# Kernel optimization log

Measured on AMD Instinct MI355X. Metric: run time of the kernel, lower is better.

Reference implementation:

```python
import jax, jax.numpy as jnp
import numpy as np
import math

H = 16
D_MODEL = 1024
D_K = D_MODEL // H
B, S = 2, 2048


def setup_inputs() -> dict:
    key = jax.random.key(0)
    ks = jax.random.split(key, 12)
    s = 1.0 / math.sqrt(D_MODEL)
    inp = {
        "Q": jax.random.normal(ks[0], (B, S, D_MODEL), jnp.float32),
        "K": jax.random.normal(ks[1], (B, S, D_MODEL), jnp.float32),
        "V": jax.random.normal(ks[2], (B, S, D_MODEL), jnp.float32),
        # causal mask: True = masked (future positions)
        "mask": jnp.triu(jnp.ones((S, S), bool), k=1)[None, None, :, :],
        "Wq": jax.random.normal(ks[3], (D_MODEL, D_MODEL), jnp.float32) * s,
        "bq": jax.random.normal(ks[4], (D_MODEL,), jnp.float32) * s,
        "Wk": jax.random.normal(ks[5], (D_MODEL, D_MODEL), jnp.float32) * s,
        "bk": jax.random.normal(ks[6], (D_MODEL,), jnp.float32) * s,
        "Wv": jax.random.normal(ks[7], (D_MODEL, D_MODEL), jnp.float32) * s,
        "bv": jax.random.normal(ks[8], (D_MODEL,), jnp.float32) * s,
        "Wo": jax.random.normal(ks[9], (D_MODEL, D_MODEL), jnp.float32) * s,
        "bo": jax.random.normal(ks[10], (D_MODEL,), jnp.float32) * s,
    }
    return inp


def reference(Q, K, V, mask, Wq, bq, Wk, bk, Wv, bv, Wo, bo):
    b, s, _ = Q.shape
    # torch Linear: y = x @ W^T + b
    q = (Q @ Wq.T + bq).reshape(b, s, H, D_K).transpose(0, 2, 1, 3)  # [b,h,s,dk]
    k = (K @ Wk.T + bk).reshape(b, s, H, D_K).transpose(0, 2, 1, 3)
    v = (V @ Wv.T + bv).reshape(b, s, H, D_K).transpose(0, 2, 1, 3)
    scores = jnp.einsum("bhqd,bhkd->bhqk", q, k) / jnp.sqrt(jnp.float32(D_K))
    scores = jnp.where(mask, jnp.float32(-1e9), scores)
    weights = jax.nn.softmax(scores, axis=-1)
    sdpa = jnp.einsum("bhqk,bhkd->bhqd", weights, v)
    sdpa = sdpa.transpose(0, 2, 1, 3).reshape(b, s, D_MODEL)
    return sdpa @ Wo.T + bo
```

## Files before the change

kernel.cpp:

```cpp
#include <hip/hip_runtime.h>
#include <hip/hip_bf16.h>
#include <stdint.h>

#define NH     16
#define DMODEL 1024
#define DKH    64
#define BATCH  2
#define SEQ    2048
#define MROWS  (BATCH * SEQ)

typedef __hip_bfloat16 bf16;
typedef __attribute__((ext_vector_type(8))) short bf16x8;
typedef __attribute__((ext_vector_type(4))) float f32x4;

#define AS3(p) ((__attribute__((address_space(3))) void*)(p))
#define AS1(p) ((const __attribute__((address_space(1))) void*)(p))

__device__ __forceinline__ f32x4 mfma16(bf16x8 a, bf16x8 b, f32x4 c) {
    return __builtin_amdgcn_mfma_f32_16x16x32_bf16(a, b, c, 0, 0, 0);
}

struct CvtArgs {
    const float* src[7];
    bf16* dst[7];
    int n[7];
};

__global__ __launch_bounds__(256) void cvt_kernel(CvtArgs a) {
    const int r = blockIdx.y;
    const int i = ((int)blockIdx.x * 256 + (int)threadIdx.x) * 4;
    if (i >= a.n[r]) return;
    const float4 v = *reinterpret_cast<const float4*>(a.src[r] + i);
    union { bf16 t[4]; uint2 u; } tu;
    tu.t[0] = __float2bfloat16(v.x);
    tu.t[1] = __float2bfloat16(v.y);
    tu.t[2] = __float2bfloat16(v.z);
    tu.t[3] = __float2bfloat16(v.w);
    *reinterpret_cast<uint2*>(reinterpret_cast<char*>(a.dst[r]) + (size_t)i * 2) = tu.u;
}

struct GemmArgs {
    const bf16* A[3];
    const bf16* W[3];
    const float* bias[3];
    void* out[3];
    int mode0;
};

__global__ __launch_bounds__(256) void gemm_bt(GemmArgs ga) {
    const int z = blockIdx.z;
    const int mode = ga.mode0 + z;
    const bf16* __restrict__ A = ga.A[z];
    const bf16* __restrict__ W = ga.W[z];
    const float* __restrict__ bias = ga.bias[z];

    __shared__ bf16 lA[128 * 64];
    __shared__ bf16 lB[128 * 64];

    const int tid = (int)threadIdx.x;
    const int w = tid >> 6;
    const int l = tid & 63;
    const int quad = l >> 4;
    const int sl = l & 15;
    const int wr = w >> 1;
    const int wc = w & 1;
    const int m0 = (int)blockIdx.x * 128;
    const int n0 = (int)blockIdx.y * 128;

    f32x4 acc[4][4];
#pragma unroll
    for (int i = 0; i < 4; ++i)
#pragma unroll
        for (int j = 0; j < 4; ++j)
            acc[i][j] = (f32x4){0.f, 0.f, 0.f, 0.f};

    for (int kt = 0; kt < 16; ++kt) {
        const int k0 = kt * 64;
        __syncthreads();
#pragma unroll
        for (int j = 0; j < 4; ++j) {
            const int row = w * 32 + j * 8 + (l >> 3);
            const int col = ((l & 7) ^ (row & 7)) * 8;
            __builtin_amdgcn_global_load_lds(AS1(A + (size_t)(m0 + row) * DMODEL + k0 + col),
                                             AS3((char*)lA + (w * 4 + j) * 1024), 16, 0, 0);
            __builtin_amdgcn_global_load_lds(AS1(W + (size_t)(n0 + row) * DMODEL + k0 + col),
                                             AS3((char*)lB + (w * 4 + j) * 1024), 16, 0, 0);
        }
        asm volatile("s_waitcnt vmcnt(0)" ::: "memory");
        __syncthreads();

        bf16x8 af[4][2], bfr[4][2];
#pragma unroll
        for (int i = 0; i < 4; ++i) {
            const int row = wr * 64 + i * 16 + sl;
#pragma unroll
            for (int ks = 0; ks < 2; ++ks) {
                const int cb = (ks * 64 + quad * 16) ^ ((row & 7) << 4);
                af[i][ks] = *reinterpret_cast<const bf16x8*>((const char*)lA + row * 128 + cb);
            }
        }
#pragma unroll
        for (int j = 0; j < 4; ++j) {
            const int row = wc * 64 + j * 16 + sl;
#pragma unroll
            for (int ks = 0; ks < 2; ++ks) {
                const int cb = (ks * 64 + quad * 16) ^ ((row & 7) << 4);
                bfr[j][ks] = *reinterpret_cast<const bf16x8*>((const char*)lB + row * 128 + cb);
            }
        }
#pragma unroll
        for (int ks = 0; ks < 2; ++ks)
#pragma unroll
            for (int i = 0; i < 4; ++i)
#pragma unroll
                for (int j = 0; j < 4; ++j)
                    acc[i][j] = mfma16(af[i][ks], bfr[j][ks], acc[i][j]);
    }

#pragma unroll
    for (int j = 0; j < 4; ++j) {
        const int n = n0 + wc * 64 + j * 16 + sl;
        const float bj = bias[n];
        const int h = n >> 6;
        const int dk = n & 63;
#pragma unroll
        for (int i = 0; i < 4; ++i) {
#pragma unroll
            for (int r = 0; r < 4; ++r) {
                const int m = m0 + wr * 64 + i * 16 + quad * 4 + r;
                const int b = m >> 11;
                const int s = m & (SEQ - 1);
                const float v = acc[i][j][r] + bj;
                if (mode == 0) {
                    ((bf16*)ga.out[z])[((size_t)(b * NH + h) * SEQ + s) * DKH + dk] =
                        __float2bfloat16(v * 0.125f);
                } else if (mode == 1) {
                    ((bf16*)ga.out[z])[((size_t)(b * NH + h) * SEQ + s) * DKH + dk] =
                        __float2bfloat16(v);
                } else if (mode == 2) {
                    ((bf16*)ga.out[z])[((size_t)(b * NH + h) * DKH + dk) * SEQ + s] =
                        __float2bfloat16(v);
                } else {
                    ((float*)ga.out[z])[(size_t)m * DMODEL + n] = v;
                }
            }
        }
    }
}

__global__ __launch_bounds__(256, 2) void attn_kernel(const bf16* __restrict__ q,
                                                      const bf16* __restrict__ k,
                                                      const bf16* __restrict__ vT,
                                                      bf16* __restrict__ o) {
    __shared__ bf16 kbuf[2][64 * 64];
    __shared__ bf16 vbuf[2][64 * 64];
    __shared__ bf16 pl[4][16][72];

    const int tid = (int)threadIdx.x;
    const int w = tid >> 6;
    const int l = tid & 63;
    const int quad = l >> 4;
    const int sl = l & 15;

    const int L = (int)blockIdx.x;
    const int j0 = L >> 3;
    const int bh = (L & 7) * 4 + (j0 >> 4);
    const int x = j0 & 15;
    const int b = bh >> 4;
    const int h = bh & 15;

    const bf16* qb = q + (size_t)bh * SEQ * DKH;
    const bf16* kb = k + (size_t)bh * SEQ * DKH;
    const bf16* vb = vT + (size_t)bh * DKH * SEQ;

    const int sq = w * 2;
    int cur = 0;

    auto stage = [&](int kv0, int buf) {
#pragma unroll
        for (int jj = 0; jj < 2; ++jj) {
            const int qq = sq + jj;
            const int row = qq * 8 + (l >> 3);
            const int col = ((l & 7) ^ (row & 7)) * 8;
            __builtin_amdgcn_global_load_lds(AS1(kb + (size_t)(kv0 + row) * DKH + col),
                                             AS3((char*)kbuf[buf] + qq * 1024), 16, 0, 0);
            __builtin_amdgcn_global_load_lds(AS1(vb + (size_t)row * SEQ + kv0 + col),
                                             AS3((char*)vbuf[buf] + qq * 1024), 16, 0, 0);
        }
    };

    for (int t = 0; t < 2; ++t) {
        const int qt = t ? (31 - x) : x;
        const int q0 = qt * 64 + w * 16;

        bf16x8 aq[2];
#pragma unroll
        for (int ks = 0; ks < 2; ++ks)
            aq[ks] = *reinterpret_cast<const bf16x8*>(
                qb + (size_t)(q0 + sl) * DKH + ks * 32 + quad * 8);

        float m_[4], ls[4];
        f32x4 o_[4];
#pragma unroll
        for (int r = 0; r < 4; ++r) { m_[r] = -3.0e38f; ls[r] = 0.f; }
#pragma unroll
        for (int dc = 0; dc < 4; ++dc) o_[dc] = (f32x4){0.f, 0.f, 0.f, 0.f};

        const int nt = qt + 1;
        stage(0, cur);

        for (int tile = 0; tile < nt; ++tile) {
            const int kv0 = tile * 64;
            asm volatile("s_waitcnt vmcnt(0)" ::: "memory");
            __syncthreads();
            if (tile + 1 < nt) stage((tile + 1) * 64, cur ^ 1);

            bf16x8 kf[4][2];
#pragma unroll
            for (int kc = 0; kc < 4; ++kc) {
                const int row = kc * 16 + sl;
#pragma unroll
                for (int ds = 0; ds < 2; ++ds) {
                    const int cb = (ds * 64 + quad * 16) ^ ((row & 7) << 4);
                    kf[kc][ds] = *reinterpret_cast<const bf16x8*>(
                        (const char*)kbuf[cur] + row * 128 + cb);
                }
            }

            f32x4 sc[4];
#pragma unroll
            for (int kc = 0; kc < 4; ++kc) sc[kc] = (f32x4){0.f, 0.f, 0.f, 0.f};
#pragma unroll
            for (int ds = 0; ds < 2; ++ds)
#pragma unroll
                for (int kc = 0; kc < 4; ++kc)
                    sc[kc] = mfma16(aq[ds], kf[kc][ds], sc[kc]);

            if (kv0 + 63 > q0) {
#pragma unroll
                for (int kc = 0; kc < 4; ++kc) {
                    const int key = kv0 + kc * 16 + sl;
#pragma unroll
                    for (int r = 0; r < 4; ++r) {
                        const int qr = q0 + quad * 4 + r;
                        if (key > qr) sc[kc][r] = -1.0e30f;
                    }
                }
            }

            float tm[4];
#pragma unroll
            for (int r = 0; r < 4; ++r)
                tm[r] = fmaxf(fmaxf(sc[0][r], sc[1][r]), fmaxf(sc[2][r], sc[3][r]));
#pragma unroll
            for (int off = 1; off < 16; off <<= 1)
#pragma unroll
                for (int r = 0; r < 4; ++r)
                    tm[r] = fmaxf(tm[r], __shfl_xor(tm[r], off, 64));

            float resc[4];
#pragma unroll
            for (int r = 0; r < 4; ++r) {
                const float mn = fmaxf(m_[r], tm[r]);
                resc[r] = __expf(m_[r] - mn);
                m_[r] = mn;
            }
            float tsum[4] = {0.f, 0.f, 0.f, 0.f};
#pragma unroll
            for (int kc = 0; kc < 4; ++kc)
#pragma unroll
                for (int r = 0; r < 4; ++r) {
                    const float p = __expf(sc[kc][r] - m_[r]);
                    sc[kc][r] = p;
                    tsum[r] += p;
                }
#pragma unroll
            for (int off = 1; off < 16; off <<= 1)
#pragma unroll
                for (int r = 0; r < 4; ++r)
                    tsum[r] += __shfl_xor(tsum[r], off, 64);
#pragma unroll
            for (int r = 0; r < 4; ++r) ls[r] = ls[r] * resc[r] + tsum[r];
#pragma unroll
            for (int dc = 0; dc < 4; ++dc)
#pragma unroll
                for (int r = 0; r < 4; ++r)
                    o_[dc][r] *= resc[r];

#pragma unroll
            for (int kc = 0; kc < 4; ++kc)
#pragma unroll
                for (int r = 0; r < 4; ++r)
                    pl[w][quad * 4 + r][kc * 16 + sl] = __float2bfloat16(sc[kc][r]);
            asm volatile("s_waitcnt lgkmcnt(0)" ::: "memory");

            bf16x8 pa[2];
#pragma unroll
            for (int ks = 0; ks < 2; ++ks)
                pa[ks] = *reinterpret_cast<const bf16x8*>(
                    reinterpret_cast<const char*>(&pl[w][0][0]) + sl * 144 + (ks * 32 + quad * 8) * 2);

            bf16x8 bv[4][2];
#pragma unroll
            for (int dc = 0; dc < 4; ++dc) {
                const int row = dc * 16 + sl;
#pragma unroll
                for (int ks = 0; ks < 2; ++ks) {
                    const int cb = (ks * 64 + quad * 16) ^ ((row & 7) << 4);
                    bv[dc][ks] = *reinterpret_cast<const bf16x8*>(
                        (const char*)vbuf[cur] + row * 128 + cb);
                }
            }
#pragma unroll
            for (int ks = 0; ks < 2; ++ks)
#pragma unroll
                for (int dc = 0; dc < 4; ++dc)
                    o_[dc] = mfma16(pa[ks], bv[dc][ks], o_[dc]);

            cur ^= 1;
        }

#pragma unroll
        for (int r = 0; r < 4; ++r) {
            const float inv = 1.f / ls[r];
            const int row = q0 + quad * 4 + r;
#pragma unroll
            for (int dc = 0; dc < 4; ++dc)
                o[((size_t)(b * SEQ + row)) * DMODEL + h * DKH + dc * 16 + sl] =
                    __float2bfloat16(o_[dc][r] * inv);
        }
    }
}

extern "C" void kernel_launch(void* const* d_in, const int* in_sizes, int n_in,
                              void* d_out, int out_size, void* d_ws, size_t ws_size,
                              hipStream_t stream) {
    const float* Q  = (const float*)d_in[0];
    const float* K  = (const float*)d_in[1];
    const float* V  = (const float*)d_in[2];
    const float* Wq = (const float*)d_in[4];
    const float* bq = (const float*)d_in[5];
    const float* Wk = (const float*)d_in[6];
    const float* bk = (const float*)d_in[7];
    const float* Wv = (const float*)d_in[8];
    const float* bv = (const float*)d_in[9];
    const float* Wo = (const float*)d_in[10];
    const float* bo = (const float*)d_in[11];

    char* ws = (char*)d_ws;
    const size_t MB = 1024 * 1024;
    bf16* Qb   = (bf16*)(ws + 0 * MB);
    bf16* Kb   = (bf16*)(ws + 8 * MB);
    bf16* Vb   = (bf16*)(ws + 16 * MB);
    bf16* Wqb  = (bf16*)(ws + 24 * MB);
    bf16* Wkb  = (bf16*)(ws + 26 * MB);
    bf16* Wvb  = (bf16*)(ws + 28 * MB);
    bf16* Wob  = (bf16*)(ws + 30 * MB);
    bf16* qh   = (bf16*)(ws + 32 * MB);
    bf16* kh   = (bf16*)(ws + 40 * MB);
    bf16* vTh  = (bf16*)(ws + 48 * MB);
    bf16* sdpa = (bf16*)(ws + 0 * MB);

    CvtArgs ca;
    ca.src[0] = Q;  ca.dst[0] = Qb;  ca.n[0] = MROWS * DMODEL;
    ca.src[1] = K;  ca.dst[1] = Kb;  ca.n[1] = MROWS * DMODEL;
    ca.src[2] = V;  ca.dst[2] = Vb;  ca.n[2] = MROWS * DMODEL;
    ca.src[3] = Wq; ca.dst[3] = Wqb; ca.n[3] = DMODEL * DMODEL;
    ca.src[4] = Wk; ca.dst[4] = Wkb; ca.n[4] = DMODEL * DMODEL;
    ca.src[5] = Wv; ca.dst[5] = Wvb; ca.n[5] = DMODEL * DMODEL;
    ca.src[6] = Wo; ca.dst[6] = Wob; ca.n[6] = DMODEL * DMODEL;
    cvt_kernel<<<dim3(4096, 7, 1), 256, 0, stream>>>(ca);

    GemmArgs g1;
    g1.A[0] = Qb; g1.W[0] = Wqb; g1.bias[0] = bq; g1.out[0] = qh;
    g1.A[1] = Kb; g1.W[1] = Wkb; g1.bias[1] = bk; g1.out[1] = kh;
    g1.A[2] = Vb; g1.W[2] = Wvb; g1.bias[2] = bv; g1.out[2] = vTh;
    g1.mode0 = 0;
    gemm_bt<<<dim3(MROWS / 128, DMODEL / 128, 3), 256, 0, stream>>>(g1);

    attn_kernel<<<dim3(512, 1, 1), 256, 0, stream>>>(qh, kh, vTh, sdpa);

    GemmArgs g2;
    g2.A[0] = sdpa; g2.W[0] = Wob; g2.bias[0] = bo; g2.out[0] = d_out;
    g2.A[1] = sdpa; g2.W[1] = Wob; g2.bias[1] = bo; g2.out[1] = d_out;
    g2.A[2] = sdpa; g2.W[2] = Wob; g2.bias[2] = bo; g2.out[2] = d_out;
    g2.mode0 = 3;
    gemm_bt<<<dim3(MROWS / 128, DMODEL / 128, 1), 256, 0, stream>>>(g2);
}
```

Baseline: 273.8 us.

## Stage 128-key KV tiles in attention and coalesce transposed V projection stores

After: 266.4 us. -2.7%, faster.

```diff
diff --git a/kernel.cpp b/kernel.cpp
--- a/kernel.cpp
+++ b/kernel.cpp
@@ -54,8 +54,9 @@
     const bf16* __restrict__ W = ga.W[z];
     const float* __restrict__ bias = ga.bias[z];
 
-    __shared__ bf16 lA[128 * 64];
-    __shared__ bf16 lB[128 * 64];
+    __shared__ __align__(16) char smem[32768];
+    bf16* lA = (bf16*)smem;
+    bf16* lB = (bf16*)(smem + 16384);
 
     const int tid = (int)threadIdx.x;
     const int w = tid >> 6;
@@ -117,6 +118,41 @@
                     acc[i][j] = mfma16(af[i][ks], bfr[j][ks], acc[i][j]);
     }
 
+    if (mode == 2) {
+        bf16* tr = (bf16*)smem;
+        const int b = m0 >> 11;
+        const int s0 = m0 & (SEQ - 1);
+        bf16* outp = (bf16*)ga.out[z];
+#pragma unroll
+        for (int jh = 0; jh < 2; ++jh) {
+            __syncthreads();
+#pragma unroll
+            for (int j2 = 0; j2 < 2; ++j2) {
+                const int j = jh * 2 + j2;
+                const int n = n0 + wc * 64 + j * 16 + sl;
+                const float bj = bias[n];
+                const int row_l = wc * 32 + j2 * 16 + sl;
+#pragma unroll
+                for (int i = 0; i < 4; ++i)
+#pragma unroll
+                    for (int r = 0; r < 4; ++r) {
+                        const int s_l = wr * 64 + i * 16 + quad * 4 + r;
+                        tr[row_l * 130 + s_l] = __float2bfloat16(acc[i][j][r] + bj);
+                    }
+            }
+            __syncthreads();
+#pragma unroll
+            for (int it = 0; it < 16; ++it) {
+                const int row_l = it * 4 + w;
+                const int wc2 = row_l >> 5;
+                const int inner = row_l & 31;
+                const int n = n0 + wc2 * 64 + jh * 32 + inner;
+                const uint32_t val = *reinterpret_cast<const uint32_t*>(&tr[row_l * 130 + l * 2]);
+                *reinterpret_cast<uint32_t*>(outp + ((size_t)(b * 1024 + n)) * SEQ + s0 + l * 2) = val;
+            }
+        }
+        return;
+    }
 #pragma unroll
     for (int j = 0; j < 4; ++j) {
         const int n = n0 + wc * 64 + j * 16 + sl;
@@ -137,9 +173,6 @@
                 } else if (mode == 1) {
                     ((bf16*)ga.out[z])[((size_t)(b * NH + h) * SEQ + s) * DKH + dk] =
                         __float2bfloat16(v);
-                } else if (mode == 2) {
-                    ((bf16*)ga.out[z])[((size_t)(b * NH + h) * DKH + dk) * SEQ + s] =
-                        __float2bfloat16(v);
                 } else {
                     ((float*)ga.out[z])[(size_t)m * DMODEL + n] = v;
                 }
@@ -152,8 +185,8 @@
                                                       const bf16* __restrict__ k,
                                                       const bf16* __restrict__ vT,
                                                       bf16* __restrict__ o) {
-    __shared__ bf16 kbuf[2][64 * 64];
-    __shared__ bf16 vbuf[2][64 * 64];
+    __shared__ bf16 kbuf[2][128 * 64];
+    __shared__ bf16 vbuf[2][64 * 128];
     __shared__ bf16 pl[4][16][72];
 
     const int tid = (int)threadIdx.x;
@@ -173,18 +206,19 @@
     const bf16* kb = k + (size_t)bh * SEQ * DKH;
     const bf16* vb = vT + (size_t)bh * DKH * SEQ;
 
-    const int sq = w * 2;
     int cur = 0;
 
     auto stage = [&](int kv0, int buf) {
 #pragma unroll
-        for (int jj = 0; jj < 2; ++jj) {
-            const int qq = sq + jj;
-            const int row = qq * 8 + (l >> 3);
-            const int col = ((l & 7) ^ (row & 7)) * 8;
-            __builtin_amdgcn_global_load_lds(AS1(kb + (size_t)(kv0 + row) * DKH + col),
+        for (int jj = 0; jj < 4; ++jj) {
+            const int qq = w * 4 + jj;
+            const int krow = qq * 8 + (l >> 3);
+            const int kcol = ((l & 7) ^ (krow & 7)) * 8;
+            __builtin_amdgcn_global_load_lds(AS1(kb + (size_t)(kv0 + krow) * DKH + kcol),
                                              AS3((char*)kbuf[buf] + qq * 1024), 16, 0, 0);
-            __builtin_amdgcn_global_load_lds(AS1(vb + (size_t)row * SEQ + kv0 + col),
+            const int dk = qq * 4 + (l >> 4);
+            const int vboff = ((l & 15) * 16) ^ ((dk & 7) << 4);
+            __builtin_amdgcn_global_load_lds(AS1(vb + (size_t)dk * SEQ + kv0 + (vboff >> 1)),
                                              AS3((char*)vbuf[buf] + qq * 1024), 16, 0, 0);
         }
     };
@@ -207,18 +241,13 @@
         for (int dc = 0; dc < 4; ++dc) o_[dc] = (f32x4){0.f, 0.f, 0.f, 0.f};
 
         const int nt = qt + 1;
-        stage(0, cur);
-
-        for (int tile = 0; tile < nt; ++tile) {
-            const int kv0 = tile * 64;
-            asm volatile("s_waitcnt vmcnt(0)" ::: "memory");
-            __syncthreads();
-            if (tile + 1 < nt) stage((tile + 1) * 64, cur ^ 1);
-
+        const int phases = (nt + 1) >> 1;
+
+        auto body = [&](int kv0, int st) {
             bf16x8 kf[4][2];
 #pragma unroll
             for (int kc = 0; kc < 4; ++kc) {
-                const int row = kc * 16 + sl;
+                const int row = st * 64 + kc * 16 + sl;
 #pragma unroll
                 for (int ds = 0; ds < 2; ++ds) {
                     const int cb = (ds * 64 + quad * 16) ^ ((row & 7) << 4);
@@ -303,12 +332,12 @@
             bf16x8 bv[4][2];
 #pragma unroll
             for (int dc = 0; dc < 4; ++dc) {
-                const int row = dc * 16 + sl;
+                const int dk = dc * 16 + sl;
 #pragma unroll
                 for (int ks = 0; ks < 2; ++ks) {
-                    const int cb = (ks * 64 + quad * 16) ^ ((row & 7) << 4);
+                    const int cb = (st * 128 + ks * 64 + quad * 16) ^ ((dk & 7) << 4);
                     bv[dc][ks] = *reinterpret_cast<const bf16x8*>(
-                        (const char*)vbuf[cur] + row * 128 + cb);
+                        (const char*)vbuf[cur] + dk * 256 + cb);
                 }
             }
 #pragma unroll
@@ -316,6 +345,17 @@
 #pragma unroll
                 for (int dc = 0; dc < 4; ++dc)
                     o_[dc] = mfma16(pa[ks], bv[dc][ks], o_[dc]);
+        };
+
+        stage(0, cur);
+        for (int p = 0; p < phases; ++p) {
+            asm volatile("s_waitcnt vmcnt(0)" ::: "memory");
+            __syncthreads();
+            if (p + 1 < phases) stage((p + 1) * 128, cur ^ 1);
+
+            const int kv0 = p * 128;
+            body(kv0, 0);
+            if (kv0 + 64 < nt * 64) body(kv0 + 64, 1);
 
             cur ^= 1;
         }
```
